# Kernel optimization log

Measured on AMD Instinct MI355X. Metric: run time of the kernel, lower is better.

Reference implementation:

```python
import jax, jax.numpy as jnp
import numpy as np
import math

B, S, D = 4, 4096, 256

def _linear(x, W, b):
    return jnp.einsum('bsd,ed->bse', x, W) + b

def _attn(x, Wq, bq, Wk, bk, Wv, bv, d):
    Q = _linear(x, Wq, bq)
    K = _linear(x, Wk, bk)
    V = _linear(x, Wv, bv)
    scores = jnp.einsum('bqd,bkd->bqk', Q, K) / math.sqrt(d)  # [B,S,S]
    w = jax.nn.softmax(scores, axis=-1)
    return jnp.einsum('bqk,bkd->bqd', w, V)

def setup_inputs() -> dict:
    key = jax.random.key(0)
    ks = jax.random.split(key, 32)
    p = {}
    p['x'] = jax.random.normal(ks[0], (B, S, D), dtype=jnp.float32)
    p['eps'] = jax.random.normal(ks[1], (B, S, D), dtype=jnp.float32)
    i = 2
    for name in ['Wq1','Wk1','Wv1','Wq2','Wk2','Wv2','Wmu','Wlv']:
        p[name] = 0.02 * jax.random.normal(ks[i], (D, D), dtype=jnp.float32); i += 1
    for name in ['bq1','bk1','bv1','bq2','bk2','bv2','bmu','blv']:
        p[name] = jnp.zeros((D,), dtype=jnp.float32)
    p['Wg'] = 0.02 * jax.random.normal(ks[i], (1, D), dtype=jnp.float32); i += 1
    p['bg'] = jnp.zeros((1,), dtype=jnp.float32)
    p['gamma'] = jnp.ones((D,), dtype=jnp.float32)
    p['beta'] = jnp.zeros((D,), dtype=jnp.float32)
    return p

def reference(x, eps, Wq1, Wk1, Wv1, Wq2, Wk2, Wv2, Wmu, Wlv,
              bq1, bk1, bv1, bq2, bk2, bv2, bmu, blv, Wg, bg, gamma, beta):
    d = x.shape[-1]
    h1 = _attn(x, Wq1, bq1, Wk1, bk1, Wv1, bv1, d)
    h2 = _attn(h1, Wq2, bq2, Wk2, bk2, Wv2, bv2, d)
    mu = _linear(h2, Wmu, bmu)
    logvar = _linear(h2, Wlv, blv)
    std = jnp.exp(0.5 * logvar)
    z = jax.nn.elu(mu + eps * std)
    p_gate = jax.nn.sigmoid(_linear(h2.mean(axis=1)[:, None, :], Wg, bg))[:, 0, 0]  # [B]
    y = x + z
    mean = y.mean(axis=-1, keepdims=True)
    var = y.var(axis=-1, keepdims=True)
    out = (y - mean) / jnp.sqrt(var + 1e-5) * gamma + beta
    return (out, mu, logvar, p_gate)
```

## Files before the change

### kernel.cpp

```cpp
#include <hip/hip_runtime.h>
#include <hip/hip_bf16.h>
#include <hip/hip_fp8.h>
#include <cstdint>
#include <cstddef>


#define S_LEN 4096
#define DMODEL 256
#define NBATCH 4

typedef __bf16 bf16;
typedef __bf16 bf16x8 __attribute__((ext_vector_type(8)));
typedef float f32x4 __attribute__((ext_vector_type(4)));
typedef float f32x16 __attribute__((ext_vector_type(16)));
typedef int i32x4 __attribute__((ext_vector_type(4)));
typedef int i32x8 __attribute__((ext_vector_type(8)));
typedef unsigned char u8;
typedef unsigned int u32;

__device__ __forceinline__ f32x4 mfma16(bf16x8 a, bf16x8 b, f32x4 c) {
  return __builtin_amdgcn_mfma_f32_16x16x32_bf16(a, b, c, 0, 0, 0);
}
__device__ __forceinline__ f32x16 mfma_mx(i32x8 a, i32x8 b, f32x16 c) {
  return __builtin_amdgcn_mfma_scale_f32_32x32x64_f8f6f4(
      a, b, c, 0, 0, 0, 0x7F7F7F7F, 0, 0x7F7F7F7F);
}
__device__ __forceinline__ i32x8 cat8(i32x4 a, i32x4 b) {
  return __builtin_shufflevector(a, b, 0, 1, 2, 3, 4, 5, 6, 7);
}

__device__ __forceinline__ void async16(const void* g, void* lds) {
  __builtin_amdgcn_global_load_lds(
      (const __attribute__((address_space(1))) unsigned int*)g,
      (__attribute__((address_space(3))) unsigned int*)lds, 16, 0, 0);
}

__device__ __forceinline__ unsigned short f2bfbits(float f) {
  return __builtin_bit_cast(unsigned short, (bf16)f);
}
__device__ __forceinline__ u8 f2fp8(float f) {
  __hip_fp8_e4m3 t(f);
  return *(u8*)&t;
}
__device__ __forceinline__ int permc(int v) {
  return (((v >> 5) & 1) << 7) + (((v >> 6) & 3) << 5) + (v & 31);
}
__device__ __forceinline__ int permc128(int v) {
  return (((v >> 5) & 1) << 6) + (((v >> 6) & 1) << 5) + (v & 31);
}

struct WPtrs { const float* p[8]; };

__global__ void cast_all_kernel(const f32x4* __restrict__ x, WPtrs wp,
                                ushort4* __restrict__ x16, ushort4* __restrict__ w16) {
  int bx = blockIdx.x, t = threadIdx.x;
  const f32x4* src;
  ushort4* dst;
  if (bx < 4096) {
    src = x + (size_t)bx * 256 + t;
    dst = x16 + (size_t)bx * 256 + t;
  } else {
    int r = bx - 4096;
    int m = r >> 6;
    int i = (r & 63) * 256 + t;
    src = (const f32x4*)wp.p[m] + i;
    dst = w16 + (size_t)m * 16384 + i;
  }
  f32x4 v = *src;
  ushort4 o;
  o.x = f2bfbits(v[0]); o.y = f2bfbits(v[1]); o.z = f2bfbits(v[2]); o.w = f2bfbits(v[3]);
  *dst = o;
}

struct GemmIO {
  const float* bias[3];
  void* out[3];
};

__global__ __launch_bounds__(256, 3) void gemm_qkv_kernel(const bf16* __restrict__ A,
                                                          const bf16* __restrict__ Wb,
                                                          GemmIO io) {
  __shared__ __align__(16) bf16 ldsA[128 * 64];
  __shared__ __align__(16) bf16 ldsB[128 * 64];
  const int t = threadIdx.x;
  const int m0 = blockIdx.x * 128;
  const int n0 = blockIdx.y * 128;
  const bf16* W = Wb + (size_t)blockIdx.z * 65536;
  const int w = t >> 6, l = t & 63, lm = l & 15, q = l >> 4;
  const int wr = (w >> 1) * 64, wc = (w & 1) * 64;

  f32x4 acc[4][4] = {};
#pragma unroll 1
  for (int it = 0; it < 4; ++it) {
    const int k0 = it * 64;
#pragma unroll
    for (int c = 0; c < 4; ++c) {
      int i = c * 256 + t;
      int r = i >> 3, c8 = (i & 7) ^ (r & 7);
      async16(A + (size_t)(m0 + r) * 256 + k0 + c8 * 8, &ldsA[i * 8]);
    }
#pragma unroll
    for (int c = 0; c < 4; ++c) {
      int i = c * 256 + t;
      int r = i >> 3, c8 = (i & 7) ^ (r & 7);
      async16(W + (size_t)(n0 + r) * 256 + k0 + c8 * 8, &ldsB[i * 8]);
    }
    __syncthreads();
#pragma unroll
    for (int ks = 0; ks < 2; ++ks) {
      bf16x8 af[4], bfr[4];
#pragma unroll
      for (int i = 0; i < 4; ++i) {
        int ra = wr + i * 16 + lm;
        af[i] = *(const bf16x8*)&ldsA[ra * 64 + ((((ks << 2) + q) ^ (ra & 7)) << 3)];
        int rb = wc + i * 16 + lm;
        bfr[i] = *(const bf16x8*)&ldsB[rb * 64 + ((((ks << 2) + q) ^ (rb & 7)) << 3)];
      }
#pragma unroll
      for (int i = 0; i < 4; ++i)
#pragma unroll
        for (int jj = 0; jj < 4; ++jj) acc[i][jj] = mfma16(af[i], bfr[jj], acc[i][jj]);
    }
    __syncthreads();
  }
  const float* bias = io.bias[blockIdx.z];
  u8* vstage = (u8*)ldsA;
  if (blockIdx.z == 2) {
#pragma unroll
    for (int jj = 0; jj < 4; ++jj) {
      int dloc = wc + jj * 16 + lm;
      float bv = bias[n0 + dloc];
#pragma unroll
      for (int i = 0; i < 4; ++i) {
        int kvb = wr + i * 16 + q * 4;
        u32 word = (u32)f2fp8(acc[i][jj][0] + bv) | ((u32)f2fp8(acc[i][jj][1] + bv) << 8) |
                   ((u32)f2fp8(acc[i][jj][2] + bv) << 16) | ((u32)f2fp8(acc[i][jj][3] + bv) << 24);
        *(u32*)&vstage[dloc * 128 + permc128(kvb)] = word;
      }
    }
    __syncthreads();
    int gtile = (m0 >> 12) * 32 + ((m0 & 4095) >> 7);
    u8* outb = (u8*)io.out[2] + ((size_t)gtile * 256 + n0) * 128;
#pragma unroll
    for (int cidx = 0; cidx < 4; ++cidx) {
      int c = cidx * 256 + t;
      ((i32x4*)outb)[c] = ((const i32x4*)vstage)[c];
    }
  } else {
    const bool isK = (blockIdx.z == 1);
#pragma unroll
    for (int jj = 0; jj < 4; ++jj) {
      int j = wc + jj * 16 + lm;
      int lc = isK ? (((j >> 5) & 1) * 64 + ((j >> 6) & 1) * 32 + (j & 31)) : j;
      float bv = bias[n0 + j];
#pragma unroll
      for (int i = 0; i < 4; ++i) {
        int rloc = wr + i * 16 + q * 4;
#pragma unroll
        for (int r = 0; r < 4; ++r)
          vstage[(rloc + r) * 128 + lc] = f2fp8(acc[i][jj][r] + bv);
      }
    }
    __syncthreads();
    u8* outz = (u8*)io.out[blockIdx.z];
    const int off = (n0 >> 7) * 64;
#pragma unroll
    for (int cidx = 0; cidx < 4; ++cidx) {
      int c = cidx * 256 + t;
      int row = c >> 3, k = c & 7;
      int gcol = isK ? ((k >> 2) * 128 + off + (k & 3) * 16) : (n0 + k * 16);
      *(i32x4*)(outz + (size_t)(m0 + row) * 256 + gcol) =
          *(const i32x4*)(vstage + row * 128 + k * 16);
    }
  }
}

__global__ __launch_bounds__(256, 3) void gemm_f_kernel(const bf16* __restrict__ A,
                                                        const bf16* __restrict__ Wb, GemmIO io) {
  __shared__ bf16 ldsA[128 * 64];
  __shared__ bf16 ldsB[128 * 64];
  const int t = threadIdx.x;
  const int m0 = blockIdx.x * 128;
  const int n0 = blockIdx.y * 128;
  const bf16* W = Wb + (size_t)blockIdx.z * 65536;
  const int w = t >> 6, l = t & 63, lm = l & 15, q = l >> 4;
  const int wr = (w >> 1) * 64, wc = (w & 1) * 64;

  f32x4 acc[4][4] = {};
#pragma unroll 1
  for (int it = 0; it < 4; ++it) {
    const int k0 = it * 64;
#pragma unroll
    for (int c = 0; c < 4; ++c) {
      int i = c * 256 + t;
      int r = i >> 3, c8 = (i & 7) ^ (r & 7);
      async16(A + (size_t)(m0 + r) * 256 + k0 + c8 * 8, &ldsA[i * 8]);
    }
#pragma unroll
    for (int c = 0; c < 4; ++c) {
      int i = c * 256 + t;
      int r = i >> 3, c8 = (i & 7) ^ (r & 7);
      async16(W + (size_t)(n0 + r) * 256 + k0 + c8 * 8, &ldsB[i * 8]);
    }
    __syncthreads();
#pragma unroll
    for (int ks = 0; ks < 2; ++ks) {
      bf16x8 af[4], bfr[4];
#pragma unroll
      for (int i = 0; i < 4; ++i) {
        int ra = wr + i * 16 + lm;
        af[i] = *(const bf16x8*)&ldsA[ra * 64 + ((((ks << 2) + q) ^ (ra & 7)) << 3)];
        int rb = wc + i * 16 + lm;
        bfr[i] = *(const bf16x8*)&ldsB[rb * 64 + ((((ks << 2) + q) ^ (rb & 7)) << 3)];
      }
#pragma unroll
      for (int i = 0; i < 4; ++i)
#pragma unroll
        for (int jj = 0; jj < 4; ++jj) acc[i][jj] = mfma16(af[i], bfr[jj], acc[i][jj]);
    }
    __syncthreads();
  }
  const float* bias = io.bias[blockIdx.z];
  float* out = (float*)io.out[blockIdx.z];
#pragma unroll
  for (int jj = 0; jj < 4; ++jj) {
    int col = n0 + wc + jj * 16 + lm;
    float bv = bias[col];
#pragma unroll
    for (int i = 0; i < 4; ++i) {
      int row = m0 + wr + i * 16 + q * 4;
#pragma unroll
      for (int r = 0; r < 4; ++r)
        out[(size_t)(row + r) * 256 + col] = acc[i][jj][r] + bv;
    }
  }
}

__global__ __launch_bounds__(1024, 4) void flash_kernel(const u8* __restrict__ Q,
                                                        const u8* __restrict__ K,
                                                        const u8* __restrict__ Vt,
                                                        bf16* __restrict__ O) {
  __shared__ __align__(16) u8 ldsK[2][128 * 256];
  __shared__ __align__(16) u8 ldsV[2][256 * 128];
  __shared__ __align__(16) u8 ldsP[2][2 * 32 * 128];
  __shared__ float lb[64];

  const int id = blockIdx.x;
  const int xcd = id & 7;
  const int b = xcd >> 1;
  const int qt = (id >> 3) + ((xcd & 1) << 5);

  const u8* Qb = Q + (size_t)b * S_LEN * 256;
  const u8* Kb = K + (size_t)b * S_LEN * 256;
  const u8* Vb = Vt + (size_t)b * 1048576;
  bf16* Ob = O + (size_t)b * S_LEN * 256;

  const int t = threadIdx.x, w = t >> 6, lane = t & 63;
  const int m31 = lane & 31, kh = lane >> 5;
  const bool prod = (w < 8);
  const float CL2 = 0.09016844005556021f;

  if (t < 64) lb[t] = 0.f;

  int kld[2], kgo[2], vld[2], vgo[2];
#pragma unroll
  for (int it = 0; it < 2; ++it) {
    int c = it * 1024 + t;
    kld[it] = c * 16;
    int kr = c >> 4, kg2 = (c & 15) ^ (kr & 7);
    kgo[it] = kr * 256 + kg2 * 16;
    vld[it] = c * 16;
    int vr = c >> 3, vg2 = (c & 7) ^ (vr & 7);
    vgo[it] = vr * 128 + vg2 * 16;
  }

  const int qg = w & 1, ks = (w >> 1) & 3;
  const int kn = ks * 32 + m31;
  const int kx = kn & 7;
  const int px = m31 & 7;
  i32x8 qf[4];
  if (prod) {
    const u8* qrow = Qb + (size_t)(qt * 64 + qg * 32 + m31) * 256 + kh * 32;
#pragma unroll
    for (int b2 = 0; b2 < 4; ++b2) qf[b2] = *(const i32x8*)(qrow + b2 * 64);
  }
  const int cw = w - 8;
  const int cqg = cw & 1, dpair = cw >> 1;
  const int vd0 = dpair * 64 + m31;
  const int vx = vd0 & 7;

  f32x16 o0 = {}, o1 = {};
  float l_w = 0.f;

#pragma unroll
  for (int it = 0; it < 2; ++it) async16(Kb + kgo[it], &ldsK[0][kld[it]]);
  __syncthreads();

#pragma unroll 1
  for (int j = 0; j <= 32; ++j) {
    if (j < 32) {
      const u8* vg = Vb + (size_t)j * 32768;
#pragma unroll
      for (int it = 0; it < 2; ++it) async16(vg + vgo[it], &ldsV[j & 1][vld[it]]);
    }
    if (j < 31) {
      const u8* kg = Kb + (size_t)(j + 1) * 128 * 256;
#pragma unroll
      for (int it = 0; it < 2; ++it) async16(kg + kgo[it], &ldsK[(j + 1) & 1][kld[it]]);
    }
    if (prod) {
      if (j < 32) {
        const u8* kb = &ldsK[j & 1][kn * 256 + kh * 128];
        f32x16 s = {};
        __builtin_amdgcn_s_setprio(1);
#pragma unroll
        for (int b2 = 0; b2 < 4; ++b2) {
          i32x4 klo = *(const i32x4*)(kb + (((2 * b2) ^ kx) << 4));
          i32x4 khi = *(const i32x4*)(kb + (((2 * b2 + 1) ^ kx) << 4));
          s = mfma_mx(cat8(klo, khi), qf[b2], s);
        }
        __builtin_amdgcn_s_setprio(0);
        float p[16];
#pragma unroll
        for (int r = 0; r < 16; ++r) {
          p[r] = __builtin_amdgcn_exp2f(s[r] * CL2);
          l_w += p[r];
        }
        u8* pst = &ldsP[j & 1][qg * 4096 + m31 * 128 + 4 * kh];
        const int cb = (ks & 1) * 4 + (ks >> 1) * 2;
#pragma unroll
        for (int g2 = 0; g2 < 4; ++g2) {
          int pk = __builtin_amdgcn_cvt_pk_fp8_f32(p[4 * g2], p[4 * g2 + 1], 0, false);
          pk = __builtin_amdgcn_cvt_pk_fp8_f32(p[4 * g2 + 2], p[4 * g2 + 3], pk, true);
          *(u32*)(pst + (((cb + (g2 >> 1)) ^ px) << 4) + ((g2 & 1) << 3)) = (u32)pk;
        }
      }
    } else {
      if (j > 0) {
        const int pb = (j - 1) & 1;
        const u8* pr = &ldsP[pb][cqg * 4096 + m31 * 128];
        const u8* v0 = &ldsV[pb][(size_t)vd0 * 128];
        const u8* v1 = v0 + 32 * 128;
        __builtin_amdgcn_s_setprio(1);
#pragma unroll
        for (int b2 = 0; b2 < 2; ++b2) {
          const int ca = 4 * kh + 2 * b2;
          i32x4 plo = *(const i32x4*)(pr + ((ca ^ px) << 4));
          i32x4 phi = *(const i32x4*)(pr + (((ca + 1) ^ px) << 4));
          i32x8 pa = cat8(plo, phi);
          i32x4 va = *(const i32x4*)(v0 + ((ca ^ vx) << 4));
          i32x4 vb2 = *(const i32x4*)(v0 + (((ca + 1) ^ vx) << 4));
          o0 = mfma_mx(pa, cat8(va, vb2), o0);
          i32x4 vc = *(const i32x4*)(v1 + ((ca ^ vx) << 4));
          i32x4 vd2 = *(const i32x4*)(v1 + (((ca + 1) ^ vx) << 4));
          o1 = mfma_mx(pa, cat8(vc, vd2), o1);
        }
        __builtin_amdgcn_s_setprio(0);
      }
    }
    __syncthreads();
  }

  if (prod) {
    l_w += __shfl_xor(l_w, 32, 64);
    if (kh == 0) atomicAdd(&lb[qg * 32 + m31], l_w);
  }
  __syncthreads();

  if (!prod) {
    bf16* ob0 = Ob + (size_t)(qt * 64 + cqg * 32) * 256 + dpair * 64;
#pragma unroll
    for (int reg = 0; reg < 16; ++reg) {
      const int row = (reg & 3) + 8 * (reg >> 2) + 4 * kh;
      float li = lb[cqg * 32 + row];
      ob0[(size_t)row * 256 + m31] = (bf16)(o0[reg] / li);
      ob0[(size_t)row * 256 + 32 + m31] = (bf16)(o1[reg] / li);
    }
  }
}

__global__ __launch_bounds__(256) void gate_partial(const bf16* __restrict__ h,
                                                    float* __restrict__ part) {
  int bb = blockIdx.y;
  const bf16* hb = h + (size_t)bb * S_LEN * 256 + (size_t)blockIdx.x * 64 * 256;
  int t = threadIdx.x;
  float acc = 0.f;
#pragma unroll 4
  for (int s = 0; s < 64; ++s) acc += (float)hb[s * 256 + t];
  part[((size_t)bb * 64 + blockIdx.x) * 256 + t] = acc;
}

__global__ __launch_bounds__(256) void gate_final(const float* __restrict__ part,
                                                  const float* __restrict__ Wg,
                                                  const float* __restrict__ bg,
                                                  float* __restrict__ pg) {
  int bb = blockIdx.x, t = threadIdx.x;
  const float* p = part + (size_t)bb * 64 * 256;
  float acc = 0.f;
#pragma unroll 4
  for (int c = 0; c < 64; ++c) acc += p[c * 256 + t];
  acc *= Wg[t] * (1.0f / 4096.0f);
  __shared__ float red[256];
  red[t] = acc;
  __syncthreads();
  if (t < 64) {
    float a = red[t] + red[t + 64] + red[t + 128] + red[t + 192];
#pragma unroll
    for (int d = 1; d < 64; d <<= 1) a += __shfl_xor(a, d, 64);
    if (t == 0) pg[bb] = 1.0f / (1.0f + __expf(-(a + bg[0])));
  }
}

__global__ __launch_bounds__(256) void epilogue_kernel(const float* __restrict__ x,
                                                       const float* __restrict__ eps,
                                                       const float* __restrict__ mu,
                                                       const float* __restrict__ lv,
                                                       const float* __restrict__ gamma,
                                                       const float* __restrict__ beta,
                                                       float* __restrict__ out) {
  size_t base = (size_t)blockIdx.x * 1024 + (threadIdx.x >> 6) * 256;
  int l = threadIdx.x & 63;
  f32x4 xv = ((const f32x4*)(x + base))[l];
  f32x4 ev = ((const f32x4*)(eps + base))[l];
  f32x4 mv = ((const f32x4*)(mu + base))[l];
  f32x4 vv = ((const f32x4*)(lv + base))[l];
  f32x4 y;
  float s = 0.f, s2 = 0.f;
#pragma unroll
  for (int c = 0; c < 4; ++c) {
    float z = mv[c] + ev[c] * __expf(0.5f * vv[c]);
    z = z > 0.f ? z : (__expf(z) - 1.f);
    float yy = xv[c] + z;
    y[c] = yy;
    s += yy;
    s2 += yy * yy;
  }
#pragma unroll
  for (int d = 1; d < 64; d <<= 1) {
    s += __shfl_xor(s, d, 64);
    s2 += __shfl_xor(s2, d, 64);
  }
  float mean = s * (1.f / 256.f);
  float var = s2 * (1.f / 256.f) - mean * mean;
  float rstd = rsqrtf(var + 1e-5f);
  f32x4 gv = ((const f32x4*)gamma)[l];
  f32x4 bv = ((const f32x4*)beta)[l];
  f32x4 o;
#pragma unroll
  for (int c = 0; c < 4; ++c) o[c] = (y[c] - mean) * rstd * gv[c] + bv[c];
  ((f32x4*)(out + base))[l] = o;
}

extern "C" void kernel_launch(void* const* d_in, const int* in_sizes, int n_in, void* d_out,
                              int out_size, void* d_ws, size_t ws_size, hipStream_t stream) {
  const float* x = (const float*)d_in[0];
  const float* eps = (const float*)d_in[1];
  const float* Wg = (const float*)d_in[18];
  const float* bg = (const float*)d_in[19];
  const float* gamma = (const float*)d_in[20];
  const float* beta = (const float*)d_in[21];

  char* ws = (char*)d_ws;
  bf16* x16 = (bf16*)(ws);
  bf16* h16 = (bf16*)(ws + 8388608);
  u8* q8 = (u8*)(ws + 25165824);
  u8* k8 = (u8*)(ws + 29360128);
  u8* vt8 = (u8*)(ws + 33554432);
  bf16* w16 = (bf16*)(ws + 37748736);
  float* gpart = (float*)(ws + 38797312);

  float* out = (float*)d_out;
  float* mu = out + 4194304;
  float* lv = out + 8388608;
  float* pg = out + 12582912;

  WPtrs wp;
  for (int i = 0; i < 8; ++i) wp.p[i] = (const float*)d_in[2 + i];
  cast_all_kernel<<<4608, 256, 0, stream>>>((const f32x4*)x, wp, (ushort4*)x16, (ushort4*)w16);

  GemmIO io1;
  io1.bias[0] = (const float*)d_in[10];
  io1.bias[1] = (const float*)d_in[11];
  io1.bias[2] = (const float*)d_in[12];
  io1.out[0] = q8; io1.out[1] = k8; io1.out[2] = vt8;
  gemm_qkv_kernel<<<dim3(128, 2, 3), 256, 0, stream>>>(x16, w16, io1);
  flash_kernel<<<256, 1024, 0, stream>>>(q8, k8, vt8, h16);

  GemmIO io2;
  io2.bias[0] = (const float*)d_in[13];
  io2.bias[1] = (const float*)d_in[14];
  io2.bias[2] = (const float*)d_in[15];
  io2.out[0] = q8; io2.out[1] = k8; io2.out[2] = vt8;
  gemm_qkv_kernel<<<dim3(128, 2, 3), 256, 0, stream>>>(h16, w16 + 3 * 65536, io2);
  flash_kernel<<<256, 1024, 0, stream>>>(q8, k8, vt8, h16);

  GemmIO io3;
  io3.bias[0] = (const float*)d_in[16];
  io3.bias[1] = (const float*)d_in[17];
  io3.bias[2] = nullptr;
  io3.out[0] = mu; io3.out[1] = lv; io3.out[2] = nullptr;
  gemm_f_kernel<<<dim3(128, 2, 2), 256, 0, stream>>>(h16, w16 + 6 * 65536, io3);

  gate_partial<<<dim3(64, 4), 256, 0, stream>>>(h16, gpart);
  gate_final<<<4, 256, 0, stream>>>(gpart, Wg, bg, pg);
  epilogue_kernel<<<4096, 256, 0, stream>>>(x, eps, mu, lv, gamma, beta, out);
}
```

Before: 271.3 us.

## Double-buffer LDS tiles in QKV and final projection GEMMs

Both projection GEMM kernels now keep two LDS buffers for the A and W tiles. The next K-slice is issued asynchronously before computing on the current one, so global-to-LDS loads overlap with MFMA work instead of sitting behind a barrier each iteration. Staging offsets are precomputed once per thread. The cost is twice the LDS per block, and the launch bound drops from 3 to 2 blocks per CU, which lowers occupancy. The GEMMs only run four K-iterations and are likely a small share of total time next to attention.

```diff
diff --git a/kernel.cpp b/kernel.cpp
--- a/kernel.cpp
+++ b/kernel.cpp
@@ -77,11 +77,11 @@
   void* out[3];
 };
 
-__global__ __launch_bounds__(256, 3) void gemm_qkv_kernel(const bf16* __restrict__ A,
+__global__ __launch_bounds__(256, 2) void gemm_qkv_kernel(const bf16* __restrict__ A,
                                                           const bf16* __restrict__ Wb,
                                                           GemmIO io) {
-  __shared__ __align__(16) bf16 ldsA[128 * 64];
-  __shared__ __align__(16) bf16 ldsB[128 * 64];
+  __shared__ __align__(16) bf16 ldsA[2][128 * 64];
+  __shared__ __align__(16) bf16 ldsB[2][128 * 64];
   const int t = threadIdx.x;
   const int m0 = blockIdx.x * 128;
   const int n0 = blockIdx.y * 128;
@@ -89,32 +89,40 @@
   const int w = t >> 6, l = t & 63, lm = l & 15, q = l >> 4;
   const int wr = (w >> 1) * 64, wc = (w & 1) * 64;
 
+  int soff[4], ldo[4];
+#pragma unroll
+  for (int c = 0; c < 4; ++c) {
+    int i = c * 256 + t;
+    int r = i >> 3, c8 = (i & 7) ^ (r & 7);
+    soff[c] = r * 256 + c8 * 8;
+    ldo[c] = i * 8;
+  }
+
+  auto STAGE = [&](int it) {
+    const int k0 = it * 64, bs = it & 1;
+#pragma unroll
+    for (int c = 0; c < 4; ++c) {
+      async16(A + (size_t)m0 * 256 + k0 + soff[c], &ldsA[bs][ldo[c]]);
+      async16(W + (size_t)n0 * 256 + k0 + soff[c], &ldsB[bs][ldo[c]]);
+    }
+  };
+
   f32x4 acc[4][4] = {};
+  STAGE(0);
+  __syncthreads();
 #pragma unroll 1
   for (int it = 0; it < 4; ++it) {
-    const int k0 = it * 64;
-#pragma unroll
-    for (int c = 0; c < 4; ++c) {
-      int i = c * 256 + t;
-      int r = i >> 3, c8 = (i & 7) ^ (r & 7);
-      async16(A + (size_t)(m0 + r) * 256 + k0 + c8 * 8, &ldsA[i * 8]);
-    }
-#pragma unroll
-    for (int c = 0; c < 4; ++c) {
-      int i = c * 256 + t;
-      int r = i >> 3, c8 = (i & 7) ^ (r & 7);
-      async16(W + (size_t)(n0 + r) * 256 + k0 + c8 * 8, &ldsB[i * 8]);
-    }
-    __syncthreads();
+    if (it < 3) STAGE(it + 1);
+    const int bs = it & 1;
 #pragma unroll
     for (int ks = 0; ks < 2; ++ks) {
       bf16x8 af[4], bfr[4];
 #pragma unroll
       for (int i = 0; i < 4; ++i) {
         int ra = wr + i * 16 + lm;
-        af[i] = *(const bf16x8*)&ldsA[ra * 64 + ((((ks << 2) + q) ^ (ra & 7)) << 3)];
+        af[i] = *(const bf16x8*)&ldsA[bs][ra * 64 + ((((ks << 2) + q) ^ (ra & 7)) << 3)];
         int rb = wc + i * 16 + lm;
-        bfr[i] = *(const bf16x8*)&ldsB[rb * 64 + ((((ks << 2) + q) ^ (rb & 7)) << 3)];
+        bfr[i] = *(const bf16x8*)&ldsB[bs][rb * 64 + ((((ks << 2) + q) ^ (rb & 7)) << 3)];
       }
 #pragma unroll
       for (int i = 0; i < 4; ++i)
@@ -175,10 +183,10 @@
   }
 }
 
-__global__ __launch_bounds__(256, 3) void gemm_f_kernel(const bf16* __restrict__ A,
+__global__ __launch_bounds__(256, 2) void gemm_f_kernel(const bf16* __restrict__ A,
                                                         const bf16* __restrict__ Wb, GemmIO io) {
-  __shared__ bf16 ldsA[128 * 64];
-  __shared__ bf16 ldsB[128 * 64];
+  __shared__ __align__(16) bf16 ldsA[2][128 * 64];
+  __shared__ __align__(16) bf16 ldsB[2][128 * 64];
   const int t = threadIdx.x;
   const int m0 = blockIdx.x * 128;
   const int n0 = blockIdx.y * 128;
@@ -186,32 +194,39 @@
   const int w = t >> 6, l = t & 63, lm = l & 15, q = l >> 4;
   const int wr = (w >> 1) * 64, wc = (w & 1) * 64;
 
+  int soff[4], ldo[4];
+#pragma unroll
+  for (int c = 0; c < 4; ++c) {
+    int i = c * 256 + t;
+    int r = i >> 3, c8 = (i & 7) ^ (r & 7);
+    soff[c] = r * 256 + c8 * 8;
+    ldo[c] = i * 8;
+  }
+  auto STAGE = [&](int it) {
+    const int k0 = it * 64, bs = it & 1;
+#pragma unroll
+    for (int c = 0; c < 4; ++c) {
+      async16(A + (size_t)m0 * 256 + k0 + soff[c], &ldsA[bs][ldo[c]]);
+      async16(W + (size_t)n0 * 256 + k0 + soff[c], &ldsB[bs][ldo[c]]);
+    }
+  };
+
   f32x4 acc[4][4] = {};
+  STAGE(0);
+  __syncthreads();
 #pragma unroll 1
   for (int it = 0; it < 4; ++it) {
-    const int k0 = it * 64;
-#pragma unroll
-    for (int c = 0; c < 4; ++c) {
-      int i = c * 256 + t;
-      int r = i >> 3, c8 = (i & 7) ^ (r & 7);
-      async16(A + (size_t)(m0 + r) * 256 + k0 + c8 * 8, &ldsA[i * 8]);
-    }
-#pragma unroll
-    for (int c = 0; c < 4; ++c) {
-      int i = c * 256 + t;
-      int r = i >> 3, c8 = (i & 7) ^ (r & 7);
-      async16(W + (size_t)(n0 + r) * 256 + k0 + c8 * 8, &ldsB[i * 8]);
-    }
-    __syncthreads();
+    if (it < 3) STAGE(it + 1);
+    const int bs = it & 1;
 #pragma unroll
     for (int ks = 0; ks < 2; ++ks) {
       bf16x8 af[4], bfr[4];
 #pragma unroll
       for (int i = 0; i < 4; ++i) {
         int ra = wr + i * 16 + lm;
-        af[i] = *(const bf16x8*)&ldsA[ra * 64 + ((((ks << 2) + q) ^ (ra & 7)) << 3)];
+        af[i] = *(const bf16x8*)&ldsA[bs][ra * 64 + ((((ks << 2) + q) ^ (ra & 7)) << 3)];
         int rb = wc + i * 16 + lm;
-        bfr[i] = *(const bf16x8*)&ldsB[rb * 64 + ((((ks << 2) + q) ^ (rb & 7)) << 3)];
+        bfr[i] = *(const bf16x8*)&ldsB[bs][rb * 64 + ((((ks << 2) + q) ^ (rb & 7)) << 3)];
       }
 #pragma unroll
       for (int i = 0; i < 4; ++i)
```

After: 281.4 us. 1.04x slower.
